# Performance work log

Measured on AMD Instinct MI355X. Metric: run time of the kernel, lower is better.

## Reference

```python
import jax, jax.numpy as jnp
import numpy as np

B, N, H, MEM, V = 512, 50, 256, 8, 40001
SCALE = 1.0 / float(np.sqrt(H))
NEG = -1e12


def sinusoid_table(n_pos, d):
    pos = np.arange(n_pos)[:, None].astype(np.float64)
    j = np.arange(d)[None, :]
    ang = pos / np.power(10000.0, 2 * (j // 2) / d)
    tab = np.zeros((n_pos, d))
    tab[:, 0::2] = np.sin(ang[:, 0::2])
    tab[:, 1::2] = np.cos(ang[:, 1::2])
    return jnp.asarray(tab, jnp.float32)

TAB = sinusoid_table(N, H)


def setup_inputs():
    key = jax.random.key(0)
    ks = jax.random.split(key, 40)
    s = 0.05
    rn = lambda k, shp, sc=s: jax.random.normal(k, shp, jnp.float32) * sc
    lengths = jax.random.randint(ks[0], (B,), 1, N + 1)
    mask = (jnp.arange(N)[None, :] < lengths[:, None]).astype(jnp.int32)
    item_flag = jax.random.randint(ks[1], (B, V - 1), 0, 2).astype(jnp.int32)
    inp = {
        'seq_emb_1': rn(ks[2], (B, N, H), 1.0),
        'seq_emb_2': rn(ks[3], (B, N, H), 1.0),
        'mask': mask,
        'item_flag': item_flag,
        # 2-layer GRU (torch layout: W_ih [3H,H], W_hh [3H,H])
        'gru_wih0': rn(ks[4], (3 * H, H)), 'gru_whh0': rn(ks[5], (3 * H, H)),
        'gru_bih0': rn(ks[6], (3 * H,)), 'gru_bhh0': rn(ks[7], (3 * H,)),
        'gru_wih1': rn(ks[8], (3 * H, H)), 'gru_whh1': rn(ks[9], (3 * H, H)),
        'gru_bih1': rn(ks[10], (3 * H,)), 'gru_bhh1': rn(ks[11], (3 * H,)),
        # attention projections ([in,out] layout, y = x @ W)
        'Wq1': rn(ks[12], (H, H)), 'Wk1': rn(ks[13], (H, H)), 'Wv1': rn(ks[14], (H, H)),
        'Wq2': rn(ks[15], (H, H)), 'Wk2': rn(ks[16], (H, H)), 'Wv2': rn(ks[17], (H, H)),
        'W_ffn1': rn(ks[18], (H, H)), 'b_ffn1': rn(ks[19], (H,)),
        'W_ffn2': rn(ks[20], (H, H)), 'b_ffn2': rn(ks[21], (H,)),
        'W_one1': rn(ks[22], (H, H)), 'b_one1': rn(ks[23], (H,)),
        'W_three1': rn(ks[24], (2 * H, 1)),
        'W_trans1': rn(ks[25], (2 * H, H)), 'b_trans1': rn(ks[26], (H,)),
        'W_tail1': rn(ks[27], (H, H)), 'b_tail1': rn(ks[28], (H,)),
        'W_tail2': rn(ks[29], (H, 2)),
        'mem_k': rn(ks[30], (1, MEM, H)), 'mem_v': rn(ks[31], (1, MEM, H)),
        'emb1': rn(ks[32], (V, H)),
    }
    return inp


def _gru_layer(x, wih, whh, bih, bhh):
    # x: [B,N,H] -> [B,N,H], h0 = 0 (torch default)
    def step(h, xt):
        gi = xt @ wih.T + bih
        gh = h @ whh.T + bhh
        ir, iz, inn = jnp.split(gi, 3, axis=-1)
        hr, hz, hn = jnp.split(gh, 3, axis=-1)
        r = jax.nn.sigmoid(ir + hr)
        z = jax.nn.sigmoid(iz + hz)
        n = jnp.tanh(inn + r * hn)
        h2 = (1.0 - z) * n + z * h
        return h2, h2
    h0 = jnp.zeros((x.shape[0], H), x.dtype)
    _, ys = jax.lax.scan(step, h0, jnp.swapaxes(x, 0, 1))
    return jnp.swapaxes(ys, 0, 1)


def _co_attention(q, k, v, mask, mem_k=None, mem_v=None):
    b = q.shape[0]
    causal = jnp.tril(jnp.ones((N, N), bool))           # [N,N]
    pad = mask.astype(bool)[:, None, :]                  # [B,1,N]
    allow_seq = causal[None, :, :] & pad                 # [B,N,N]
    if mem_k is not None:
        k = jnp.concatenate([jnp.broadcast_to(mem_k, (b, MEM, H)), k], axis=1)
        v = jnp.concatenate([jnp.broadcast_to(mem_v, (b, MEM, H)), v], axis=1)
        mem_ok = jnp.ones((b, N, MEM), bool)             # memory keys always visible
        allow = jnp.concatenate([mem_ok, allow_seq], axis=-1)
    else:
        allow = allow_seq
    att = jnp.einsum('bqh,bkh->bqk', q, k) * SCALE
    att = jax.nn.softmax(jnp.where(allow, att, NEG), axis=-1)
    return jnp.einsum('bqk,bkh->bqh', att, v) * mask[:, :, None].astype(q.dtype)


def reference(seq_emb_1, seq_emb_2, mask, item_flag,
              gru_wih0, gru_whh0, gru_bih0, gru_bhh0,
              gru_wih1, gru_whh1, gru_bih1, gru_bhh1,
              Wq1, Wk1, Wv1, Wq2, Wk2, Wv2,
              W_ffn1, b_ffn1, W_ffn2, b_ffn2,
              W_one1, b_one1, W_three1, W_trans1, b_trans1,
              W_tail1, b_tail1, W_tail2, mem_k, mem_v, emb1):
    b = mask.shape[0]
    mf = mask[:, :, None].astype(jnp.float32)
    # 2-layer GRU on stream 2
    s2 = _gru_layer(seq_emb_2, gru_wih0, gru_whh0, gru_bih0, gru_bhh0)
    s2 = _gru_layer(s2, gru_wih1, gru_whh1, gru_bih1, gru_bhh1)
    last = jnp.sum(mask, axis=1) - 1                     # last valid index
    sr_l_1 = seq_emb_1[jnp.arange(b), last]              # [B,H]
    q1_1 = sr_l_1 @ W_one1 + b_one1 + TAB[0]
    se1 = seq_emb_1 * mf
    # positional encoding indexed by |pos - last_idx|
    flag = jnp.abs(jnp.arange(N, dtype=jnp.int32)[None, :] - last[:, None].astype(jnp.int32))
    pe = TAB[flag]                                       # [B,N,H]
    q1 = se1 @ Wq1 + pe
    k1 = se1 @ Wk1 + pe
    v1 = se1 @ Wv1 + pe
    att1 = _co_attention(q1, k1, v1, mask) @ W_ffn1 + b_ffn1
    se2 = s2 * mf
    k2 = se2 @ Wk2
    v2 = se2 @ Wv2
    att2 = _co_attention(q1, k2, v2, mask, mem_k, mem_v) @ W_ffn2 + b_ffn2
    att = jax.nn.relu(att1 + att2)
    alpha = jnp.concatenate([att, jnp.broadcast_to(q1_1[:, None, :], att.shape)], axis=-1) @ W_three1
    alpha = jax.nn.softmax(jnp.where(mf > 0, alpha, NEG), axis=1)  # [B,N,1]
    sess = jnp.sum(alpha * se1 * mf, axis=1)
    sess = jnp.concatenate([sess, sr_l_1], axis=1) @ W_trans1 + b_trans1
    item_emb = emb1[1:]                                  # [V-1,H]
    score = sess @ item_emb.T                            # [B,V-1]
    fl = item_flag.astype(bool)
    score_in = jax.nn.softmax(jnp.where(fl, score, NEG), axis=-1)
    score_ex = jax.nn.softmax(jnp.where(fl, NEG, score), axis=-1)
    beta = jax.nn.softmax(jax.nn.relu(sess @ W_tail1 + b_tail1) @ W_tail2, axis=-1)  # [B,2]
    boundary = jnp.mean(jnp.abs(beta[:, 0] - beta[:, 1]))
    final = score_in * beta[:, 0:1] + score_ex * beta[:, 1:2]
    return final[:, None, :], boundary
```

## Files before the change

### kernel.cpp

```cpp
#include <hip/hip_runtime.h>
#include <hip/hip_bf16.h>
#include <cstdint>
#include <cstddef>

#define Bsz 512
#define Nsq 50
#define Hd  256
#define VM1 40000
static constexpr float SCALE_C = 0.0625f;
static constexpr float NEG_C   = -1.0e12f;

typedef __attribute__((ext_vector_type(8))) short bf16x8;
typedef __attribute__((ext_vector_type(4))) float f32x4;

__device__ __forceinline__ float sigmoidf_(float x) { return 1.0f / (1.0f + __expf(-x)); }
__device__ __forceinline__ float tanh_fast(float x) {
  float t = fminf(fmaxf(2.0f * x, -60.0f), 60.0f);
  float e = __expf(t);
  return (e - 1.0f) / (e + 1.0f);
}
__device__ __forceinline__ ushort f2b(float x) {
  union { float f; uint32_t u; } c; c.f = x;
  uint32_t r = (c.u + 0x7fffu + ((c.u >> 16) & 1u)) >> 16;
  return (ushort)r;
}

__global__ void build_tab(float* __restrict__ TAB) {
  int idx = blockIdx.x * 256 + threadIdx.x;
  int pos = idx >> 8, j = idx & 255;
  int pair = j >> 1;
  float expo = (2.0f * (float)pair) / 256.0f;
  float inv = powf(10000.0f, -expo);
  float ang = (float)pos * inv;
  TAB[idx] = (j & 1) ? cosf(ang) : sinf(ang);
}

__global__ __launch_bounds__(256) void last_srl_kernel(const int* __restrict__ mask,
    const float* __restrict__ seq1, int* __restrict__ lastp, float* __restrict__ srl) {
  int b = blockIdx.x, tid = threadIdx.x;
  __shared__ int ls;
  if (tid == 0) {
    int c = 0;
    for (int t = 0; t < Nsq; ++t) c += mask[b * Nsq + t];
    ls = c - 1;
    lastp[b] = c - 1;
  }
  __syncthreads();
  srl[b * Hd + tid] = seq1[((size_t)b * Nsq + ls) * Hd + tid];
}

template <int BT, int BIAS>
__global__ __launch_bounds__(256) void gemm_tile(const float* __restrict__ A,
    const float* __restrict__ B, const float* __restrict__ bias,
    float* __restrict__ C, int M, int N, int K) {
  __shared__ float As[16][132];
  __shared__ float Bs[16][68];
  int bm = blockIdx.y * 128, bn = blockIdx.x * 64;
  int tid = threadIdx.x;
  int tm = (tid >> 4) << 3;
  int tn = (tid & 15) << 2;
  float acc[8][4] = {};
  for (int k0 = 0; k0 < K; k0 += 16) {
#pragma unroll
    for (int u = 0; u < 8; ++u) {
      int i = tid + u * 256;
      int kk = i & 15, m = i >> 4;
      As[kk][m] = A[(size_t)(bm + m) * K + (k0 + kk)];
    }
#pragma unroll
    for (int u = 0; u < 4; ++u) {
      int i = tid + u * 256;
      if (BT) {
        int kk = i & 15, n = i >> 4;
        Bs[kk][n] = B[(size_t)(bn + n) * K + (k0 + kk)];
      } else {
        int n = i & 63, kk = i >> 6;
        Bs[kk][n] = B[(size_t)(k0 + kk) * N + (bn + n)];
      }
    }
    __syncthreads();
#pragma unroll
    for (int kk = 0; kk < 16; ++kk) {
      float a[8], bb[4];
#pragma unroll
      for (int r = 0; r < 8; ++r) a[r] = As[kk][tm + r];
#pragma unroll
      for (int c = 0; c < 4; ++c) bb[c] = Bs[kk][tn + c];
#pragma unroll
      for (int r = 0; r < 8; ++r)
#pragma unroll
        for (int c = 0; c < 4; ++c) acc[r][c] += a[r] * bb[c];
    }
    __syncthreads();
  }
#pragma unroll
  for (int r = 0; r < 8; ++r) {
    size_t row = (size_t)(bm + tm + r) * N + bn;
#pragma unroll
    for (int c = 0; c < 4; ++c) {
      float v = acc[r][c];
      if (BIAS) v += bias[bn + tn + c];
      C[row + tn + c] = v;
    }
  }
}

template <int BT, int BIAS>
__global__ __launch_bounds__(256) void mfma_gemm(const ushort* __restrict__ A,
    const ushort* __restrict__ B, const float* __restrict__ bias,
    float* __restrict__ C, int M, int N, int K) {
  __shared__ ushort Asm[128][40];
  __shared__ ushort Bsm[128][40];
  int tid = threadIdx.x;
  int bm = blockIdx.y * 128, bn = blockIdx.x * 128;
  int lane = tid & 63, wave = tid >> 6;
  int quad = lane >> 4, l16 = lane & 15;
  int wm = (wave >> 1) * 64, wn = (wave & 1) * 64;
  f32x4 acc[4][4] = {};
  for (int k0 = 0; k0 < K; k0 += 32) {
#pragma unroll
    for (int u = 0; u < 2; ++u) {
      int idx = tid + u * 256;
      int r = idx >> 2, kc = (idx & 3) * 8;
      uint4 v = *(const uint4*)(A + (size_t)(bm + r) * K + k0 + kc);
      *(uint4*)&Asm[r][kc] = v;
    }
    if (BT) {
#pragma unroll
      for (int u = 0; u < 2; ++u) {
        int idx = tid + u * 256;
        int r = idx >> 2, kc = (idx & 3) * 8;
        uint4 v = make_uint4(0u, 0u, 0u, 0u);
        if (bn + r < N) v = *(const uint4*)(B + (size_t)(bn + r) * K + k0 + kc);
        *(uint4*)&Bsm[r][kc] = v;
      }
    } else {
#pragma unroll
      for (int u = 0; u < 8; ++u) {
        int idx = tid + u * 256;
        int n2 = (idx & 63) * 2, kk = idx >> 6;
        uint v = *(const uint*)(B + (size_t)(k0 + kk) * N + bn + n2);
        Bsm[n2][kk] = (ushort)(v & 0xffffu);
        Bsm[n2 + 1][kk] = (ushort)(v >> 16);
      }
    }
    __syncthreads();
    bf16x8 af[4], bfr[4];
#pragma unroll
    for (int f = 0; f < 4; ++f) af[f] = *(const bf16x8*)&Asm[wm + f * 16 + l16][quad * 8];
#pragma unroll
    for (int f = 0; f < 4; ++f) bfr[f] = *(const bf16x8*)&Bsm[wn + f * 16 + l16][quad * 8];
#pragma unroll
    for (int mf = 0; mf < 4; ++mf)
#pragma unroll
      for (int nf = 0; nf < 4; ++nf)
        acc[mf][nf] = __builtin_amdgcn_mfma_f32_16x16x32_bf16(af[mf], bfr[nf], acc[mf][nf], 0, 0, 0);
    __syncthreads();
  }
#pragma unroll
  for (int mf = 0; mf < 4; ++mf) {
#pragma unroll
    for (int r = 0; r < 4; ++r) {
      int row = bm + wm + mf * 16 + quad * 4 + r;
      size_t rowo = (size_t)row * N;
#pragma unroll
      for (int nf = 0; nf < 4; ++nf) {
        int col = bn + wn + nf * 16 + l16;
        if (col < N) {
          float v = acc[mf][nf][r];
          if (BIAS) v += bias[col];
          C[rowo + col] = v;
        }
      }
    }
  }
}

__global__ void cast_f2b_k(const float* __restrict__ s, ushort* __restrict__ d, int n4) {
  int i = blockIdx.x * 256 + threadIdx.x;
  if (i >= n4) return;
  const float4 v = ((const float4*)s)[i];
  ushort4 o; o.x = f2b(v.x); o.y = f2b(v.y); o.z = f2b(v.z); o.w = f2b(v.w);
  ((ushort4*)d)[i] = o;
}

struct Cast7 { const float* s[7]; ushort* d[7]; };
__global__ void cast7_k(Cast7 p) {
  int m = blockIdx.y;
  int i = blockIdx.x * 256 + threadIdx.x;
  const float4 v = ((const float4*)p.s[m])[i];
  ushort4 o; o.x = f2b(v.x); o.y = f2b(v.y); o.z = f2b(v.z); o.w = f2b(v.w);
  ((ushort4*)p.d[m])[i] = o;
}

__global__ void add_tab0(float* __restrict__ q) {
  int idx = blockIdx.x * 256 + threadIdx.x;
  q[idx] += (float)(threadIdx.x & 1);
}

__global__ void mask_mul_dual(const float* __restrict__ x, const int* __restrict__ m,
                              float* __restrict__ y, ushort* __restrict__ yb) {
  int idx = blockIdx.x * 256 + threadIdx.x;
  float v = m[idx >> 8] ? x[idx] : 0.0f;
  y[idx] = v;
  yb[idx] = f2b(v);
}

__global__ void add_pe3(float* __restrict__ q, float* __restrict__ k, float* __restrict__ v,
                        const float* __restrict__ TAB, const int* __restrict__ lastp) {
  int idx = blockIdx.x * 256 + threadIdx.x;
  int j = idx & 255, bt = idx >> 8;
  int b = bt / Nsq, t = bt - b * Nsq;
  int d = abs(t - lastp[b]);
  float pe = TAB[d * 256 + j];
  q[idx] += pe; k[idx] += pe; v[idx] += pe;
}

__global__ void relu_add(float* __restrict__ a, const float* __restrict__ b) {
  int idx = blockIdx.x * 256 + threadIdx.x;
  a[idx] = fmaxf(a[idx] + b[idx], 0.0f);
}

__global__ __launch_bounds__(512, 2) void gru_mfma8_kernel(const float* __restrict__ gi,
    const ushort* __restrict__ whhb, const float* __restrict__ bhh,
    ushort* __restrict__ ysb, const int* __restrict__ mask) {
  __shared__ ushort hbf[16][264];
  __shared__ float  ghs[2][768];
  int tid = threadIdx.x;
  int lane = tid & 63, wave = tid >> 6;
  int quad = lane >> 4, l16 = lane & 15;
  int s0 = blockIdx.x * 2;

  for (int i = tid; i < 16 * 264 / 2; i += 512) ((uint*)hbf)[i] = 0u;

  bf16x8 bw[48];
  const ushort* wb = whhb + (size_t)(wave * 96 + l16) * 256 + quad * 8;
#pragma unroll
  for (int f = 0; f < 48; ++f) {
    int nf = f >> 3, kf = f & 7;
    bw[f] = *(const bf16x8*)(wb + nf * (16 * 256) + kf * 32);
  }

  int d = tid & 255, sh = tid >> 8;
  float bh0 = bhh[d], bh1 = bhh[256 + d], bh2 = bhh[512 + d];
  const float* gib = gi + (size_t)(s0 + sh) * Nsq * 768;
  float g0 = gib[d], g1 = gib[256 + d], g2 = gib[512 + d];
  float hreg = 0.0f;
  __syncthreads();

  for (int t = 0; t < Nsq; ++t) {
    int tn = (t + 1 < Nsq) ? t + 1 : t;
    float p0 = gib[tn * 768 + d], p1 = gib[tn * 768 + 256 + d], p2 = gib[tn * 768 + 512 + d];

    f32x4 acc[6] = {};
#pragma unroll
    for (int kf = 0; kf < 8; ++kf) {
      bf16x8 a = *(const bf16x8*)&hbf[l16][kf * 32 + quad * 8];
#pragma unroll
      for (int nf = 0; nf < 6; ++nf)
        acc[nf] = __builtin_amdgcn_mfma_f32_16x16x32_bf16(a, bw[nf * 8 + kf], acc[nf], 0, 0, 0);
    }
    if (quad == 0) {
#pragma unroll
      for (int nf = 0; nf < 6; ++nf) {
        int n = wave * 96 + nf * 16 + l16;
        ghs[0][n] = acc[nf][0];
        ghs[1][n] = acc[nf][1];
      }
    }
    __syncthreads();

    {
      float rr = sigmoidf_(g0 + ghs[sh][d] + bh0);
      float zz = sigmoidf_(g1 + ghs[sh][256 + d] + bh1);
      float nn = tanh_fast(g2 + rr * (ghs[sh][512 + d] + bh2));
      float h2 = (1.0f - zz) * nn + zz * hreg;
      hreg = h2;
      hbf[sh][d] = f2b(h2);
      float ov = h2;
      if (mask) ov = mask[(s0 + sh) * Nsq + t] ? h2 : 0.0f;
      ysb[((size_t)(s0 + sh) * Nsq + t) * 256 + d] = f2b(ov);
    }
    g0 = p0; g1 = p1; g2 = p2;
    __syncthreads();
  }
}

template <int NMEM>
__global__ __launch_bounds__(256) void attn_mfma(const float* __restrict__ q1,
    const float* __restrict__ kseq, const float* __restrict__ vseq,
    const float* __restrict__ kmem, const float* __restrict__ vmem,
    const int* __restrict__ mask, ushort* __restrict__ out) {
  constexpr int NK = NMEM + Nsq;
  __shared__ ushort KV[64][264];
  __shared__ float Ss[64][66];
  __shared__ ushort Ps[64][72];
  __shared__ int msk[64];
  int tid = threadIdx.x;
  int lane = tid & 63, wave = tid >> 6;
  int quad = lane >> 4, l16 = lane & 15;
  int b = blockIdx.x;

  if (tid < 64) msk[tid] = (tid < Nsq) ? mask[b * Nsq + tid] : 0;

#pragma unroll
  for (int it = 0; it < 16; ++it) {
    int idx = tid + it * 256;
    int r = idx >> 6, c4 = (idx & 63) * 4;
    float4 v = make_float4(0.f, 0.f, 0.f, 0.f);
    if (r < Nsq) v = *(const float4*)(q1 + ((size_t)(b * Nsq + r)) * 256 + c4);
    ushort4 o; o.x = f2b(v.x); o.y = f2b(v.y); o.z = f2b(v.z); o.w = f2b(v.w);
    *(ushort4*)&KV[r][c4] = o;
  }
  __syncthreads();
  bf16x8 qa[8];
#pragma unroll
  for (int kf = 0; kf < 8; ++kf)
    qa[kf] = *(const bf16x8*)&KV[wave * 16 + l16][kf * 32 + quad * 8];
  __syncthreads();

#pragma unroll
  for (int it = 0; it < 16; ++it) {
    int idx = tid + it * 256;
    int r = idx >> 6, c4 = (idx & 63) * 4;
    float4 v = make_float4(0.f, 0.f, 0.f, 0.f);
    if (r < NK) {
      const float* src = (NMEM > 0 && r < NMEM)
          ? (kmem + (size_t)r * 256 + c4)
          : (kseq + ((size_t)(b * Nsq + (r - NMEM))) * 256 + c4);
      v = *(const float4*)src;
    }
    ushort4 o; o.x = f2b(v.x); o.y = f2b(v.y); o.z = f2b(v.z); o.w = f2b(v.w);
    *(ushort4*)&KV[r][c4] = o;
  }
  __syncthreads();

  {
    f32x4 acc[4] = {};
#pragma unroll
    for (int kf = 0; kf < 8; ++kf) {
#pragma unroll
      for (int nf = 0; nf < 4; ++nf) {
        bf16x8 bf = *(const bf16x8*)&KV[nf * 16 + l16][kf * 32 + quad * 8];
        acc[nf] = __builtin_amdgcn_mfma_f32_16x16x32_bf16(qa[kf], bf, acc[nf], 0, 0, 0);
      }
    }
#pragma unroll
    for (int nf = 0; nf < 4; ++nf)
#pragma unroll
      for (int r = 0; r < 4; ++r)
        Ss[wave * 16 + quad * 4 + r][nf * 16 + l16] = acc[nf][r];
  }
  __syncthreads();

#pragma unroll
  for (int it = 0; it < 16; ++it) {
    int idx = tid + it * 256;
    int r = idx >> 6, c4 = (idx & 63) * 4;
    float4 v = make_float4(0.f, 0.f, 0.f, 0.f);
    if (r < NK) {
      const float* src = (NMEM > 0 && r < NMEM)
          ? (vmem + (size_t)r * 256 + c4)
          : (vseq + ((size_t)(b * Nsq + (r - NMEM))) * 256 + c4);
      v = *(const float4*)src;
    }
    ushort4 o; o.x = f2b(v.x); o.y = f2b(v.y); o.z = f2b(v.z); o.w = f2b(v.w);
    *(ushort4*)&KV[r][c4] = o;
  }
  if (tid < 64) {
    int t = tid;
    if (t < Nsq) {
      float m = -1e30f;
      for (int j = 0; j < NK; ++j) {
        bool ok = (j < NMEM) || (((j - NMEM) <= t) && (msk[j - NMEM] != 0));
        if (ok) m = fmaxf(m, Ss[t][j] * SCALE_C);
      }
      float sum = 0.0f;
      for (int j = 0; j < NK; ++j) {
        bool ok = (j < NMEM) || (((j - NMEM) <= t) && (msk[j - NMEM] != 0));
        if (ok) sum += __expf(Ss[t][j] * SCALE_C - m);
      }
      float inv = 1.0f / sum;
      for (int j = 0; j < 64; ++j) {
        float p = 0.0f;
        if (j < NK) {
          bool ok = (j < NMEM) || (((j - NMEM) <= t) && (msk[j - NMEM] != 0));
          if (ok) p = __expf(Ss[t][j] * SCALE_C - m) * inv;
        }
        Ps[t][j] = f2b(p);
      }
    } else {
      for (int j = 0; j < 64; ++j) Ps[t][j] = 0;
    }
  }
  __syncthreads();

  {
    f32x4 o[4][4] = {};
#pragma unroll
    for (int kf = 0; kf < 2; ++kf) {
      bf16x8 pa[4];
#pragma unroll
      for (int mf = 0; mf < 4; ++mf)
        pa[mf] = *(const bf16x8*)&Ps[mf * 16 + l16][kf * 32 + quad * 8];
#pragma unroll
      for (int nf = 0; nf < 4; ++nf) {
        int h = wave * 64 + nf * 16 + l16;
        ushort e0 = KV[kf * 32 + quad * 8 + 0][h];
        ushort e1 = KV[kf * 32 + quad * 8 + 1][h];
        ushort e2 = KV[kf * 32 + quad * 8 + 2][h];
        ushort e3 = KV[kf * 32 + quad * 8 + 3][h];
        ushort e4 = KV[kf * 32 + quad * 8 + 4][h];
        ushort e5 = KV[kf * 32 + quad * 8 + 5][h];
        ushort e6 = KV[kf * 32 + quad * 8 + 6][h];
        ushort e7 = KV[kf * 32 + quad * 8 + 7][h];
        bf16x8 vb = {(short)e0, (short)e1, (short)e2, (short)e3,
                     (short)e4, (short)e5, (short)e6, (short)e7};
#pragma unroll
        for (int mf = 0; mf < 4; ++mf)
          o[mf][nf] = __builtin_amdgcn_mfma_f32_16x16x32_bf16(pa[mf], vb, o[mf][nf], 0, 0, 0);
      }
    }
#pragma unroll
    for (int mf = 0; mf < 4; ++mf) {
#pragma unroll
      for (int r = 0; r < 4; ++r) {
        int t = mf * 16 + quad * 4 + r;
        if (t < Nsq) {
          int zero = (msk[t] == 0);
#pragma unroll
          for (int nf = 0; nf < 4; ++nf) {
            int h = wave * 64 + nf * 16 + l16;
            float val = zero ? 0.0f : o[mf][nf][r];
            out[((size_t)(b * Nsq + t)) * 256 + h] = f2b(val);
          }
        }
      }
    }
  }
}

__global__ __launch_bounds__(256) void alpha_sess_kernel(const float* __restrict__ att,
    const float* __restrict__ W3, const float* __restrict__ q11,
    const float* __restrict__ se1, const int* __restrict__ mask,
    const float* __restrict__ srl, float* __restrict__ sesscat) {
  int b = blockIdx.x, tid = threadIdx.x;
  __shared__ float red[256];
  __shared__ float ash[50];
  red[tid] = q11[b * Hd + tid] * W3[256 + tid];
  __syncthreads();
  for (int s = 128; s; s >>= 1) { if (tid < s) red[tid] += red[tid + s]; __syncthreads(); }
  float cq = red[0];
  float aval = 0.0f;
  if (tid < 50) {
    float s = cq;
    const float* ar = att + ((size_t)b * Nsq + tid) * Hd;
    for (int hh = 0; hh < 256; ++hh) s += ar[hh] * W3[hh];
    aval = mask[b * Nsq + tid] ? s : NEG_C;
  }
  if (tid < 64) {
    float s = (tid < 50) ? aval : NEG_C;
    float m = s;
    for (int off = 32; off; off >>= 1) m = fmaxf(m, __shfl_xor(m, off));
    float e = expf(s - m);
    float sum = e;
    for (int off = 32; off; off >>= 1) sum += __shfl_xor(sum, off);
    if (tid < 50) ash[tid] = e / sum;
  }
  __syncthreads();
  float acc = 0.0f;
  const float* se = se1 + (size_t)b * Nsq * Hd;
  for (int t = 0; t < Nsq; ++t) acc += ash[t] * se[t * 256 + tid];
  sesscat[(size_t)b * 512 + tid] = acc;
  sesscat[(size_t)b * 512 + 256 + tid] = srl[b * Hd + tid];
}

__global__ __launch_bounds__(256) void beta_kernel(const float* __restrict__ sess2,
    const float* __restrict__ Wt1, const float* __restrict__ bt1,
    const float* __restrict__ Wt2, float* __restrict__ beta, float* __restrict__ bnd) {
  int b = blockIdx.x, tid = threadIdx.x;
  __shared__ float xs[256];
  __shared__ float r0[256], r1[256];
  xs[tid] = sess2[b * Hd + tid];
  __syncthreads();
  float hsum = bt1[tid];
  for (int k = 0; k < 256; ++k) hsum += xs[k] * Wt1[k * 256 + tid];
  float hid = fmaxf(hsum, 0.0f);
  r0[tid] = hid * Wt2[tid * 2 + 0];
  r1[tid] = hid * Wt2[tid * 2 + 1];
  __syncthreads();
  for (int s = 128; s; s >>= 1) {
    if (tid < s) { r0[tid] += r0[tid + s]; r1[tid] += r1[tid + s]; }
    __syncthreads();
  }
  if (tid == 0) {
    float t0 = r0[0], t1 = r1[0];
    float m = fmaxf(t0, t1);
    float e0 = expf(t0 - m), e1 = expf(t1 - m);
    float bb0 = e0 / (e0 + e1), bb1 = e1 / (e0 + e1);
    beta[b * 2] = bb0; beta[b * 2 + 1] = bb1;
    atomicAdd(bnd, fabsf(bb0 - bb1) * (1.0f / 512.0f));
  }
}

__global__ __launch_bounds__(1024) void score_final_fused(float* __restrict__ score,
    const int* __restrict__ flag, const float* __restrict__ beta) {
  int b = blockIdx.x, tid = threadIdx.x;
  float4* sr = (float4*)(score + (size_t)b * VM1);
  const int4* fr = (const int4*)(flag + (size_t)b * VM1);
  constexpr int NV = VM1 / 4;
  constexpr int NW = (NV + 7) / 8;

  __shared__ uint bits[NW];
  __shared__ float red[1024], red2[1024];

  for (int i = tid; i < NW; i += 1024) bits[i] = 0u;
  __syncthreads();

  float mi = -INFINITY, me = -INFINITY;
  for (int i = tid; i < NV; i += 1024) {
    float4 s = sr[i];
    int4 f = fr[i];
    uint nib = (f.x ? 1u : 0u) | (f.y ? 2u : 0u) | (f.z ? 4u : 0u) | (f.w ? 8u : 0u);
    if (nib) atomicOr(&bits[i >> 3], nib << ((i & 7) * 4));
    if (f.x) mi = fmaxf(mi, s.x); else me = fmaxf(me, s.x);
    if (f.y) mi = fmaxf(mi, s.y); else me = fmaxf(me, s.y);
    if (f.z) mi = fmaxf(mi, s.z); else me = fmaxf(me, s.z);
    if (f.w) mi = fmaxf(mi, s.w); else me = fmaxf(me, s.w);
  }
  red[tid] = mi; red2[tid] = me;
  __syncthreads();
  for (int s = 512; s; s >>= 1) {
    if (tid < s) { red[tid] = fmaxf(red[tid], red[tid + s]); red2[tid] = fmaxf(red2[tid], red2[tid + s]); }
    __syncthreads();
  }
  float Mi = red[0], Me = red2[0];
  __syncthreads();

  float si = 0.0f, se = 0.0f;
  for (int i = tid; i < NV; i += 1024) {
    float4 s = sr[i];
    uint nib = bits[i >> 3] >> ((i & 7) * 4);
    float e0 = __expf(s.x - ((nib & 1u) ? Mi : Me));
    float e1 = __expf(s.y - ((nib & 2u) ? Mi : Me));
    float e2 = __expf(s.z - ((nib & 4u) ? Mi : Me));
    float e3 = __expf(s.w - ((nib & 8u) ? Mi : Me));
    si += ((nib & 1u) ? e0 : 0.0f) + ((nib & 2u) ? e1 : 0.0f)
        + ((nib & 4u) ? e2 : 0.0f) + ((nib & 8u) ? e3 : 0.0f);
    se += ((nib & 1u) ? 0.0f : e0) + ((nib & 2u) ? 0.0f : e1)
        + ((nib & 4u) ? 0.0f : e2) + ((nib & 8u) ? 0.0f : e3);
  }
  red[tid] = si; red2[tid] = se;
  __syncthreads();
  for (int s = 512; s; s >>= 1) {
    if (tid < s) { red[tid] += red[tid + s]; red2[tid] += red2[tid + s]; }
    __syncthreads();
  }
  float c0 = beta[b * 2] / red[0];
  float c1 = beta[b * 2 + 1] / red2[0];
  __syncthreads();

  for (int i = tid; i < NV; i += 1024) {
    float4 s = sr[i];
    uint nib = bits[i >> 3] >> ((i & 7) * 4);
    s.x = ((nib & 1u) ? c0 : c1) * __expf(s.x - ((nib & 1u) ? Mi : Me));
    s.y = ((nib & 2u) ? c0 : c1) * __expf(s.y - ((nib & 2u) ? Mi : Me));
    s.z = ((nib & 4u) ? c0 : c1) * __expf(s.z - ((nib & 4u) ? Mi : Me));
    s.w = ((nib & 8u) ? c0 : c1) * __expf(s.w - ((nib & 8u) ? Mi : Me));
    sr[i] = s;
  }
}

extern "C" void kernel_launch(void* const* d_in, const int* in_sizes, int n_in,
                              void* d_out, int out_size, void* d_ws, size_t ws_size,
                              hipStream_t stream) {
  const float* seq1  = (const float*)d_in[0];
  const float* seq2  = (const float*)d_in[1];
  const int*   mask  = (const int*)d_in[2];
  const int*   iflag = (const int*)d_in[3];
  const float* wih0  = (const float*)d_in[4];
  const float* whh0  = (const float*)d_in[5];
  const float* bih0  = (const float*)d_in[6];
  const float* bhh0  = (const float*)d_in[7];
  const float* wih1  = (const float*)d_in[8];
  const float* whh1  = (const float*)d_in[9];
  const float* bih1  = (const float*)d_in[10];
  const float* bhh1  = (const float*)d_in[11];
  const float* Wq1   = (const float*)d_in[12];
  const float* Wk1   = (const float*)d_in[13];
  const float* Wv1   = (const float*)d_in[14];
  const float* Wk2   = (const float*)d_in[16];
  const float* Wv2   = (const float*)d_in[17];
  const float* Wffn1 = (const float*)d_in[18];
  const float* bffn1 = (const float*)d_in[19];
  const float* Wffn2 = (const float*)d_in[20];
  const float* bffn2 = (const float*)d_in[21];
  const float* Wone  = (const float*)d_in[22];
  const float* bone  = (const float*)d_in[23];
  const float* W3    = (const float*)d_in[24];
  const float* Wtr   = (const float*)d_in[25];
  const float* btr   = (const float*)d_in[26];
  const float* Wt1   = (const float*)d_in[27];
  const float* bt1   = (const float*)d_in[28];
  const float* Wt2   = (const float*)d_in[29];
  const float* memk  = (const float*)d_in[30];
  const float* memv  = (const float*)d_in[31];
  const float* emb1  = (const float*)d_in[32];
  float* out = (float*)d_out;

  char* wsb = (char*)d_ws;
  float*  TAB    = (float*)(wsb + 0);
  int*    lastp  = (int*)  (wsb + 51200);
  float*  srl    = (float*)(wsb + 53248);
  float*  q11    = (float*)(wsb + 577536);
  ushort* whh0b  = (ushort*)(wsb + 1101824);
  ushort* whh1b  = (ushort*)(wsb + 1888256);
  ushort* wih0b  = (ushort*)(wsb + 2674688);
  ushort* wih1b  = (ushort*)(wsb + 3067904);
  ushort* w7b    = (ushort*)(wsb + 3461120);
  ushort* bufS   = (ushort*)(wsb + 4378624);
  float*  se1    = (float*)(wsb + 17485824);
  ushort* se1b   = (ushort*)(wsb + 43700224);
  float*  giQ    = (float*)(wsb + 56807424);
  float*  kv2a   = (float*)(wsb + 135450624);
  float*  kv2b   = (float*)(wsb + 161665024);
  ushort* ao1b   = (ushort*)(wsb + 187879424);
  ushort* ao2b   = (ushort*)(wsb + 200986624);

  float* gi = giQ;
  float* q1 = giQ;
  float* k1 = giQ + 6553600;
  float* v1 = giQ + 13107200;
  ushort* embB    = (ushort*)giQ;
  float*  sesscat = (float*)((char*)giQ + 20480000);
  float*  sess2   = (float*)((char*)giQ + 21528576);
  ushort* sess2b  = (ushort*)((char*)giQ + 22052864);
  float*  betab   = (float*)((char*)giQ + 22315008);
  float*  stats   = (float*)((char*)giQ + 22319104);
  float*  bnd     = out + (size_t)Bsz * VM1;

  ushort* Wq1b = w7b;              ushort* Wk1b = w7b + 65536;
  ushort* Wv1b = w7b + 131072;     ushort* Wk2b = w7b + 196608;
  ushort* Wv2b = w7b + 262144;     ushort* Wf1b = w7b + 327680;
  ushort* Wf2b = w7b + 393216;

  build_tab<<<50, 256, 0, stream>>>(TAB);
  last_srl_kernel<<<Bsz, 256, 0, stream>>>(mask, seq1, lastp, srl);
  gemm_tile<0, 1><<<dim3(4, 4), 256, 0, stream>>>(srl, Wone, bone, q11, 512, 256, 256);
  add_tab0<<<512, 256, 0, stream>>>(q11);

  cast_f2b_k<<<6400, 256, 0, stream>>>(seq2, bufS, 1638400);
  cast_f2b_k<<<192, 256, 0, stream>>>(wih0, wih0b, 49152);
  cast_f2b_k<<<192, 256, 0, stream>>>(wih1, wih1b, 49152);
  cast_f2b_k<<<192, 256, 0, stream>>>(whh0, whh0b, 49152);
  cast_f2b_k<<<192, 256, 0, stream>>>(whh1, whh1b, 49152);
  Cast7 c7;
  c7.s[0] = Wq1; c7.s[1] = Wk1; c7.s[2] = Wv1; c7.s[3] = Wk2; c7.s[4] = Wv2;
  c7.s[5] = Wffn1; c7.s[6] = Wffn2;
  c7.d[0] = Wq1b; c7.d[1] = Wk1b; c7.d[2] = Wv1b; c7.d[3] = Wk2b; c7.d[4] = Wv2b;
  c7.d[5] = Wf1b; c7.d[6] = Wf2b;
  cast7_k<<<dim3(64, 7), 256, 0, stream>>>(c7);

  mfma_gemm<1, 1><<<dim3(6, 200), 256, 0, stream>>>(bufS, wih0b, bih0, gi, 25600, 768, 256);
  gru_mfma8_kernel<<<256, 512, 0, stream>>>(gi, whh0b, bhh0, bufS, nullptr);
  mfma_gemm<1, 1><<<dim3(6, 200), 256, 0, stream>>>(bufS, wih1b, bih1, gi, 25600, 768, 256);
  gru_mfma8_kernel<<<256, 512, 0, stream>>>(gi, whh1b, bhh1, bufS, mask);

  mask_mul_dual<<<25600, 256, 0, stream>>>(seq1, mask, se1, se1b);

  mfma_gemm<0, 0><<<dim3(2, 200), 256, 0, stream>>>(bufS, Wk2b, nullptr, kv2a, 25600, 256, 256);
  mfma_gemm<0, 0><<<dim3(2, 200), 256, 0, stream>>>(bufS, Wv2b, nullptr, kv2b, 25600, 256, 256);
  mfma_gemm<0, 0><<<dim3(2, 200), 256, 0, stream>>>(se1b, Wq1b, nullptr, q1, 25600, 256, 256);
  mfma_gemm<0, 0><<<dim3(2, 200), 256, 0, stream>>>(se1b, Wk1b, nullptr, k1, 25600, 256, 256);
  mfma_gemm<0, 0><<<dim3(2, 200), 256, 0, stream>>>(se1b, Wv1b, nullptr, v1, 25600, 256, 256);
  add_pe3<<<25600, 256, 0, stream>>>(q1, k1, v1, TAB, lastp);

  attn_mfma<0><<<Bsz, 256, 0, stream>>>(q1, k1, v1, nullptr, nullptr, mask, ao1b);
  attn_mfma<8><<<Bsz, 256, 0, stream>>>(q1, kv2a, kv2b, memk, memv, mask, ao2b);
  mfma_gemm<0, 1><<<dim3(2, 200), 256, 0, stream>>>(ao1b, Wf1b, bffn1, kv2a, 25600, 256, 256);
  mfma_gemm<0, 1><<<dim3(2, 200), 256, 0, stream>>>(ao2b, Wf2b, bffn2, kv2b, 25600, 256, 256);
  relu_add<<<25600, 256, 0, stream>>>(kv2a, kv2b);

  alpha_sess_kernel<<<Bsz, 256, 0, stream>>>(kv2a, W3, q11, se1, mask, srl, sesscat);
  gemm_tile<0, 1><<<dim3(4, 4), 256, 0, stream>>>(sesscat, Wtr, btr, sess2, 512, 256, 512);
  cast_f2b_k<<<128, 256, 0, stream>>>(sess2, sess2b, 32768);

  hipMemsetAsync(bnd, 0, 4, stream);
  beta_kernel<<<Bsz, 256, 0, stream>>>(sess2, Wt1, bt1, Wt2, betab, bnd);
  cast_f2b_k<<<10000, 256, 0, stream>>>(emb1 + 256, embB, 2560000);
  mfma_gemm<1, 0><<<dim3(313, 4), 256, 0, stream>>>(sess2b, embB, nullptr, out, 512, VM1, 256);
  score_final_fused<<<Bsz, 1024, 0, stream>>>(out, iflag, betab);

  (void)in_sizes; (void)n_in; (void)out_size; (void)ws_size;
}
```

Measured before the change: 978.2 us.

## Remap GRU gate columns per wave to drop one barrier per timestep

Result: no change. 963.6 us (-1.5%).

```diff
diff --git a/kernel.cpp b/kernel.cpp
--- a/kernel.cpp
+++ b/kernel.cpp
@@ -224,64 +224,73 @@
 __global__ __launch_bounds__(512, 2) void gru_mfma8_kernel(const float* __restrict__ gi,
     const ushort* __restrict__ whhb, const float* __restrict__ bhh,
     ushort* __restrict__ ysb, const int* __restrict__ mask) {
-  __shared__ ushort hbf[16][264];
-  __shared__ float  ghs[2][768];
+  __shared__ ushort hbf[2][16][264];
+  __shared__ float  gsc[8][2][3][32];
   int tid = threadIdx.x;
   int lane = tid & 63, wave = tid >> 6;
   int quad = lane >> 4, l16 = lane & 15;
   int s0 = blockIdx.x * 2;
 
-  for (int i = tid; i < 16 * 264 / 2; i += 512) ((uint*)hbf)[i] = 0u;
+  for (int i = tid; i < 2 * 16 * 264 / 2; i += 512) ((uint*)hbf)[i] = 0u;
 
   bf16x8 bw[48];
-  const ushort* wb = whhb + (size_t)(wave * 96 + l16) * 256 + quad * 8;
 #pragma unroll
   for (int f = 0; f < 48; ++f) {
     int nf = f >> 3, kf = f & 7;
-    bw[f] = *(const bf16x8*)(wb + nf * (16 * 256) + kf * 32);
-  }
-
-  int d = tid & 255, sh = tid >> 8;
+    int row = (nf >> 1) * 256 + wave * 32 + (nf & 1) * 16 + l16;
+    bw[f] = *(const bf16x8*)(whhb + (size_t)row * 256 + kf * 32 + quad * 8);
+  }
+
+  int s = lane >> 5, dloc = lane & 31;
+  int d = wave * 32 + dloc;
   float bh0 = bhh[d], bh1 = bhh[256 + d], bh2 = bhh[512 + d];
-  const float* gib = gi + (size_t)(s0 + sh) * Nsq * 768;
-  float g0 = gib[d], g1 = gib[256 + d], g2 = gib[512 + d];
+  const float* gib = gi + (size_t)(s0 + s) * Nsq * 768 + d;
+  float g0 = gib[0], g1 = gib[256], g2 = gib[512];
   float hreg = 0.0f;
-  __syncthreads();
-
+  const int* mrow = mask + (s0 + s) * Nsq;
+  ushort* yrow = ysb + ((size_t)(s0 + s) * Nsq) * 256 + d;
+  __syncthreads();
+
+  int cur = 0;
   for (int t = 0; t < Nsq; ++t) {
     int tn = (t + 1 < Nsq) ? t + 1 : t;
-    float p0 = gib[tn * 768 + d], p1 = gib[tn * 768 + 256 + d], p2 = gib[tn * 768 + 512 + d];
+    float p0 = gib[tn * 768], p1 = gib[tn * 768 + 256], p2 = gib[tn * 768 + 512];
 
     f32x4 acc[6] = {};
 #pragma unroll
     for (int kf = 0; kf < 8; ++kf) {
-      bf16x8 a = *(const bf16x8*)&hbf[l16][kf * 32 + quad * 8];
+      bf16x8 a = *(const bf16x8*)&hbf[cur][l16][kf * 32 + quad * 8];
 #pragma unroll
       for (int nf = 0; nf < 6; ++nf)
         acc[nf] = __builtin_amdgcn_mfma_f32_16x16x32_bf16(a, bw[nf * 8 + kf], acc[nf], 0, 0, 0);
     }
     if (quad == 0) {
 #pragma unroll
-      for (int nf = 0; nf < 6; ++nf) {
-        int n = wave * 96 + nf * 16 + l16;
-        ghs[0][n] = acc[nf][0];
-        ghs[1][n] = acc[nf][1];
-      }
-    }
-    __syncthreads();
+      for (int g = 0; g < 3; ++g)
+#pragma unroll
+        for (int j = 0; j < 2; ++j) {
+          gsc[wave][0][g][j * 16 + l16] = acc[g * 2 + j][0];
+          gsc[wave][1][g][j * 16 + l16] = acc[g * 2 + j][1];
+        }
+    }
+    __builtin_amdgcn_sched_barrier(0);
 
     {
-      float rr = sigmoidf_(g0 + ghs[sh][d] + bh0);
-      float zz = sigmoidf_(g1 + ghs[sh][256 + d] + bh1);
-      float nn = tanh_fast(g2 + rr * (ghs[sh][512 + d] + bh2));
+      float ghr = gsc[wave][s][0][dloc];
+      float ghz = gsc[wave][s][1][dloc];
+      float ghn = gsc[wave][s][2][dloc];
+      float rr = sigmoidf_(g0 + ghr + bh0);
+      float zz = sigmoidf_(g1 + ghz + bh1);
+      float nn = tanh_fast(g2 + rr * (ghn + bh2));
       float h2 = (1.0f - zz) * nn + zz * hreg;
       hreg = h2;
-      hbf[sh][d] = f2b(h2);
+      hbf[cur ^ 1][s][d] = f2b(h2);
       float ov = h2;
-      if (mask) ov = mask[(s0 + sh) * Nsq + t] ? h2 : 0.0f;
-      ysb[((size_t)(s0 + sh) * Nsq + t) * 256 + d] = f2b(ov);
+      if (mask) ov = mrow[t] ? h2 : 0.0f;
+      yrow[t * 256] = f2b(ov);
     }
     g0 = p0; g1 = p1; g2 = p2;
+    cur ^= 1;
     __syncthreads();
   }
 }
```
